# Kernel tuning notes

Hardware: AMD Instinct MI355X
Metric: run time of the kernel (lower is better)

The kernel has to match this reference:

```python
import jax, jax.numpy as jnp
import numpy as np

B, N, H, E, L = 64, 100, 128, 128, 3  # batch, nodes, node_hidden, edge_hidden, gcn layers


def setup_inputs() -> dict:
    key = jax.random.key(0)
    ks = jax.random.split(key, 12)
    s = 0.05
    return dict(
        node=jax.random.normal(ks[0], (B, N, 2), jnp.float32),
        demand=jax.random.uniform(ks[1], (B, N), jnp.float32),
        dis=jax.random.uniform(ks[2], (B, N, N), jnp.float32),
        Wn0=jax.random.normal(ks[3], (3, H), jnp.float32) * s,
        bn0=jnp.zeros((H,), jnp.float32),
        Ws=jax.random.normal(ks[4], (L, H, H), jnp.float32) * s,
        Wngh=jax.random.normal(ks[5], (L, H, H), jnp.float32) * s,
        We=jax.random.normal(ks[6], (E,), jnp.float32) * s,
        be=jnp.zeros((E,), jnp.float32),
        Wih=jax.random.normal(ks[7], (2, H, 3 * H), jnp.float32) * s,
        Whh=jax.random.normal(ks[8], (2, H, 3 * H), jnp.float32) * s,
        bih=jnp.zeros((2, 3 * H), jnp.float32),
        bhh=jnp.zeros((2, 3 * H), jnp.float32),
        Wq=jax.random.normal(ks[9], (H, H), jnp.float32) * s,
        Wc=jax.random.normal(ks[10], (E, 2), jnp.float32) * s,
        bc=jnp.zeros((2,), jnp.float32),
    )


def _gru(xin, h, Wih, Whh, bih, bhh):
    gi = xin @ Wih + bih
    gh = h @ Whh + bhh
    ir, iz, inn = jnp.split(gi, 3, -1)
    hr, hz, hn = jnp.split(gh, 3, -1)
    r = jax.nn.sigmoid(ir + hr)
    z = jax.nn.sigmoid(iz + hz)
    n = jnp.tanh(inn + r * hn)
    return (1.0 - z) * n + z * h


def _decode(x, Wih, Whh, bih, bhh, Wq, sample, key):
    b, n, h = x.shape
    scale = 1.0 / np.sqrt(h).astype(np.float32)

    def step(carry, _):
        last, hid, k = carry
        emb = x[jnp.arange(b), last]                      # [b,h]
        h0 = _gru(emb, hid[0], Wih[0], Whh[0], bih[0], bhh[0])
        h1 = _gru(h0, hid[1], Wih[1], Whh[1], bih[1], bhh[1])
        logits = jnp.einsum('bh,bnh->bn', h1 @ Wq, x) * scale
        logp = jax.nn.log_softmax(logits, -1)
        k, sk = jax.random.split(k)
        if sample:
            ind = jax.random.categorical(sk, logits)
        else:
            ind = jnp.argmax(logits, -1)
        ind = ind.astype(jnp.int32)
        chosen = jnp.take_along_axis(logp, ind[:, None], 1)[:, 0]
        return (ind, jnp.stack([h0, h1]), k), (ind, chosen)

    init = (jnp.zeros((b,), jnp.int32), jnp.zeros((2, b, h), x.dtype), key)
    _, (inds, lps) = jax.lax.scan(step, init, None, length=n - 1)
    solution = jnp.concatenate([jnp.zeros((b, 1), jnp.int32), inds.T], axis=1)  # depot 0 first
    return lps.T, solution  # logprob [b,n-1], solution [b,n]


def _count_dist(sol, dis):
    bidx = jnp.arange(sol.shape[0])[:, None]
    return dis[bidx, sol[:, :-1], sol[:, 1:]].sum(axis=1, keepdims=True)  # [b,1]


def reference(node, demand, dis, Wn0, bn0, Ws, Wngh, We, be, Wih, Whh, bih, bhh, Wq, Wc, bc):
    # --- GCN encoder ---
    h = jax.nn.relu(jnp.concatenate([node, demand[..., None]], -1) @ Wn0 + bn0)  # [B,N,H]
    A = jax.nn.softmax(-dis, -1)  # distance-based soft adjacency
    for l in range(Ws.shape[0]):
        h = jax.nn.relu(h @ Ws[l] + jnp.einsum('bij,bjh->bih', A, h @ Wngh[l]))
    e = jax.nn.relu(dis[..., None] * We + be)  # [B,N,N,E]

    key = jax.random.key(42)
    k1, _ = jax.random.split(key)
    sample_logprob, sample_solution = _decode(h, Wih, Whh, bih, bhh, Wq, True, k1)
    sample_distance = _count_dist(sample_solution, dis)
    _, greedy_solution = _decode(h, Wih, Whh, bih, bhh, Wq, False, k1)
    greedy_distance = _count_dist(greedy_solution, dis)

    predict_matrix = jax.nn.softmax(e @ Wc + bc, -1)  # [B,N,N,2]

    b, n = h.shape[0], h.shape[1]
    bidx = jnp.arange(b)[:, None]
    greedy_solution_matrix = (
        jnp.zeros((b, n, n), jnp.int32)
        .at[bidx, greedy_solution[:, :-1], greedy_solution[:, 1:]]
        .set(1)
    )
    return (sample_logprob, sample_distance, greedy_distance, predict_matrix, greedy_solution_matrix)
```

## Files before the change

### kernel.cpp

```cpp
#include <hip/hip_runtime.h>
#include <math.h>

#define BB 64
#define NN 100
#define HH 128
#define T3 384

#define O0 0
#define O1 6336
#define O2 6400
#define O3 6464
#define O4 1286464

#define TINYF 1.17549435e-38f

__device__ __forceinline__ unsigned rotl32(unsigned x, int d) {
    return (x << d) | (x >> (32 - d));
}

__device__ __forceinline__ void tf2x32(unsigned ks0, unsigned ks1,
                                       unsigned x0, unsigned x1,
                                       unsigned& o0, unsigned& o1) {
    unsigned ks2 = ks0 ^ ks1 ^ 0x1BD11BDAu;
    x0 += ks0; x1 += ks1;
    x0 += x1; x1 = rotl32(x1, 13); x1 ^= x0;
    x0 += x1; x1 = rotl32(x1, 15); x1 ^= x0;
    x0 += x1; x1 = rotl32(x1, 26); x1 ^= x0;
    x0 += x1; x1 = rotl32(x1, 6);  x1 ^= x0;
    x0 += ks1; x1 += ks2 + 1u;
    x0 += x1; x1 = rotl32(x1, 17); x1 ^= x0;
    x0 += x1; x1 = rotl32(x1, 29); x1 ^= x0;
    x0 += x1; x1 = rotl32(x1, 16); x1 ^= x0;
    x0 += x1; x1 = rotl32(x1, 24); x1 ^= x0;
    x0 += ks2; x1 += ks0 + 2u;
    x0 += x1; x1 = rotl32(x1, 13); x1 ^= x0;
    x0 += x1; x1 = rotl32(x1, 15); x1 ^= x0;
    x0 += x1; x1 = rotl32(x1, 26); x1 ^= x0;
    x0 += x1; x1 = rotl32(x1, 6);  x1 ^= x0;
    x0 += ks0; x1 += ks1 + 3u;
    x0 += x1; x1 = rotl32(x1, 17); x1 ^= x0;
    x0 += x1; x1 = rotl32(x1, 29); x1 ^= x0;
    x0 += x1; x1 = rotl32(x1, 16); x1 ^= x0;
    x0 += x1; x1 = rotl32(x1, 24); x1 ^= x0;
    x0 += ks1; x1 += ks2 + 4u;
    x0 += x1; x1 = rotl32(x1, 13); x1 ^= x0;
    x0 += x1; x1 = rotl32(x1, 15); x1 ^= x0;
    x0 += x1; x1 = rotl32(x1, 26); x1 ^= x0;
    x0 += x1; x1 = rotl32(x1, 6);  x1 ^= x0;
    x0 += ks2; x1 += ks0 + 5u;
    o0 = x0; o1 = x1;
}

__device__ __forceinline__ float gumbel_f(unsigned k0, unsigned k1, unsigned f) {
    unsigned o0, o1;
    tf2x32(k0, k1, 0u, f, o0, o1);
    unsigned bits = o0 ^ o1;
    float u01 = __uint_as_float((bits >> 9) | 0x3F800000u) - 1.0f;
    float u = fmaxf(TINYF, u01 * (1.0f - TINYF) + TINYF);
    return -logf(-logf(u));
}


__global__ void k_embed(const float* __restrict__ node, const float* __restrict__ demand,
                        const float* __restrict__ Wn0, const float* __restrict__ bn0,
                        float* __restrict__ h) {
    int idx = blockIdx.x * 256 + threadIdx.x;
    if (idx >= BB * NN * HH) return;
    int r = idx >> 7, c = idx & 127;
    float v = node[r * 2] * Wn0[c] + node[r * 2 + 1] * Wn0[128 + c]
            + demand[r] * Wn0[256 + c] + bn0[c];
    h[idx] = fmaxf(v, 0.0f);
}

__global__ void k_adj(const float* __restrict__ dis, float* __restrict__ A) {
    int row = blockIdx.x;
    const float* d = dis + row * NN;
    int l = threadIdx.x;
    float v0 = (l < NN) ? -d[l] : -__builtin_inff();
    float v1 = (l + 64 < NN) ? -d[l + 64] : -__builtin_inff();
    float m = fmaxf(v0, v1);
    for (int off = 32; off > 0; off >>= 1) m = fmaxf(m, __shfl_xor(m, off));
    float e0 = (l < NN) ? expf(v0 - m) : 0.0f;
    float e1 = (l + 64 < NN) ? expf(v1 - m) : 0.0f;
    float s = e0 + e1;
    for (int off = 32; off > 0; off >>= 1) s += __shfl_xor(s, off);
    float inv = 1.0f / s;
    if (l < NN) A[row * NN + l] = e0 * inv;
    if (l + 64 < NN) A[row * NN + l + 64] = e1 * inv;
}

__global__ void k_hw(const float* __restrict__ h, const float* __restrict__ W,
                     float* __restrict__ out) {
    __shared__ float hs[8 * 128];
    int block_row = blockIdx.x * 8;
    int tid = threadIdx.x;
    int col = tid & 127;
    int rg = tid >> 7;
    for (int i = tid; i < 8 * 128; i += 256) hs[i] = h[block_row * 128 + i];
    __syncthreads();
    float acc[4] = {0.f, 0.f, 0.f, 0.f};
    for (int k = 0; k < 128; k++) {
        float w = W[k * 128 + col];
#pragma unroll
        for (int r = 0; r < 4; r++) acc[r] += hs[(rg + 2 * r) * 128 + k] * w;
    }
#pragma unroll
    for (int r = 0; r < 4; r++)
        out[(block_row + rg + 2 * r) * 128 + col] = acc[r];
}

__global__ void k_mm384(const float* __restrict__ h, const float* __restrict__ W,
                        const float* __restrict__ bias, float* __restrict__ out) {
    __shared__ float hs[8 * 128];
    int block_row = blockIdx.x * 8;
    int tid = threadIdx.x;
    int col = blockIdx.y * 128 + (tid & 127);
    int rg = tid >> 7;
    for (int i = tid; i < 8 * 128; i += 256) hs[i] = h[block_row * 128 + i];
    __syncthreads();
    float acc[4] = {0.f, 0.f, 0.f, 0.f};
    for (int k = 0; k < 128; k++) {
        float w = W[k * 384 + col];
#pragma unroll
        for (int r = 0; r < 4; r++) acc[r] += hs[(rg + 2 * r) * 128 + k] * w;
    }
    float b = bias[col];
#pragma unroll
    for (int r = 0; r < 4; r++)
        out[(block_row + rg + 2 * r) * 384 + col] = acc[r] + b;
}

__global__ void k_transpose128(const float* __restrict__ Wq, float* __restrict__ WqT) {
    int i = blockIdx.x * 256 + threadIdx.x;
    if (i >= 128 * 128) return;
    int k = i >> 7, c = i & 127;
    WqT[k * 128 + c] = Wq[c * 128 + k];
}

__global__ void k_agg(const float* __restrict__ h, const float* __restrict__ Ws,
                      const float* __restrict__ A, const float* __restrict__ hw,
                      float* __restrict__ out) {
    __shared__ float hs[4 * 128];
    __shared__ float As[4 * 100];
    int b = blockIdx.x / 25;
    int i0 = (blockIdx.x % 25) * 4;
    int tid = threadIdx.x;
    int col = tid & 127;
    int rg = tid >> 7;
    int rowbase = b * NN + i0;
    for (int idx = tid; idx < 4 * 128; idx += 256) hs[idx] = h[rowbase * 128 + idx];
    for (int idx = tid; idx < 4 * 100; idx += 256) As[idx] = A[rowbase * 100 + idx];
    __syncthreads();
    float acc0 = 0.f, acc1 = 0.f;
    for (int k = 0; k < 128; k++) {
        float w = Ws[k * 128 + col];
        acc0 += hs[rg * 128 + k] * w;
        acc1 += hs[(rg + 2) * 128 + k] * w;
    }
    const float* hwb = hw + b * NN * 128;
    for (int j = 0; j < NN; j++) {
        float v = hwb[j * 128 + col];
        acc0 += As[rg * 100 + j] * v;
        acc1 += As[(rg + 2) * 100 + j] * v;
    }
    out[(rowbase + rg) * 128 + col]     = fmaxf(acc0, 0.0f);
    out[(rowbase + rg + 2) * 128 + col] = fmaxf(acc1, 0.0f);
}

__global__ void k_predict(const float* __restrict__ dis, const float* __restrict__ We,
                          const float* __restrict__ be, const float* __restrict__ Wc,
                          const float* __restrict__ bc, float* __restrict__ out3) {
    __shared__ float sWe[128], sbe[128], sc0[128], sc1[128];
    int tid = threadIdx.x;
    if (tid < 128) {
        sWe[tid] = We[tid];
        sbe[tid] = be[tid];
        sc0[tid] = Wc[tid * 2];
        sc1[tid] = Wc[tid * 2 + 1];
    }
    __syncthreads();
    float b0 = bc[0], b1 = bc[1];
    for (int pos = blockIdx.x * 256 + tid; pos < BB * NN * NN; pos += gridDim.x * 256) {
        float d = dis[pos];
        float a0 = b0, a1 = b1;
        for (int k = 0; k < 128; k++) {
            float e = fmaxf(d * sWe[k] + sbe[k], 0.0f);
            a0 += e * sc0[k];
            a1 += e * sc1[k];
        }
        float m = fmaxf(a0, a1);
        float p0 = expf(a0 - m), p1 = expf(a1 - m);
        float inv = 1.0f / (p0 + p1);
        out3[pos * 2]     = p0 * inv;
        out3[pos * 2 + 1] = p1 * inv;
    }
}

__global__ void k_zero(float* __restrict__ p, int n) {
    int i = blockIdx.x * 256 + threadIdx.x;
    if (i < n) p[i] = 0.0f;
}

__global__ __launch_bounds__(768) void k_decode2(
    const float* __restrict__ P0,
    const float* __restrict__ Z,
    const float* __restrict__ dis,
    const float* __restrict__ Wih,
    const float* __restrict__ Whh,
    const float* __restrict__ bih,
    const float* __restrict__ bhh,
    float* __restrict__ out) {
    __shared__ float Zs[NN * 129];
    __shared__ float h0s[128], h1s[128];
    __shared__ float gi0s[T3];
    __shared__ float pg0[2 * T3];
    __shared__ float gi1s[T3], gh1s[T3];
    __shared__ float sbhh0[T3], sbih1[T3], sbhh1[T3];
    __shared__ float pl[4 * NN];
    __shared__ float logits[NN];
    __shared__ float s_m, s_s;
    __shared__ int s_ind;

    const int tid = threadIdx.x;
    const int b = blockIdx.x >> 1;
    const int greedy = blockIdx.x & 1;
    const float SCALE = 0.08838834764831845f;

    const float* Whh0 = Whh;
    const float* Wih1 = Wih + 128 * T3;
    const float* Whh1 = Whh + 128 * T3;

    for (int idx = tid; idx < NN * 128; idx += 768) {
        int r = idx >> 7, c = idx & 127;
        Zs[r * 129 + c] = Z[(b * NN + r) * 128 + c];
    }
    if (tid < T3) {
        sbhh0[tid] = bhh[tid];
        sbih1[tid] = bih[T3 + tid];
        sbhh1[tid] = bhh[T3 + tid];
    }
    if (tid < 128) { h0s[tid] = 0.0f; h1s[tid] = 0.0f; }

    unsigned kk0, kk1;
    tf2x32(0u, 42u, 0u, 0u, kk0, kk1);

    int last = 0;
    float dist = 0.0f;
    __syncthreads();

    for (int t = 0; t < NN - 1; t++) {
        unsigned sk0, sk1, nk0, nk1;
        tf2x32(kk0, kk1, 0u, 1u, sk0, sk1);
        tf2x32(kk0, kk1, 0u, 0u, nk0, nk1);
        kk0 = nk0; kk1 = nk1;

        {
            const float* P0row = P0 + (b * NN + last) * T3;
            if (tid < T3) {
                int j = tid;
                float acc = 0.0f;
#pragma unroll 16
                for (int k = 0; k < 64; k++) acc += h0s[k] * Whh0[k * T3 + j];
                pg0[j] = acc;
                gi0s[j] = P0row[j];
            } else {
                int j = tid - T3;
                float acc = 0.0f;
#pragma unroll 16
                for (int k = 64; k < 128; k++) acc += h0s[k] * Whh0[k * T3 + j];
                pg0[T3 + j] = acc;
            }
        }
        __syncthreads();

        if (tid < 128) {
            float ghr = pg0[tid] + pg0[T3 + tid] + sbhh0[tid];
            float ghz = pg0[tid + 128] + pg0[T3 + tid + 128] + sbhh0[tid + 128];
            float ghn = pg0[tid + 256] + pg0[T3 + tid + 256] + sbhh0[tid + 256];
            float r = 1.0f / (1.0f + expf(-(gi0s[tid] + ghr)));
            float z = 1.0f / (1.0f + expf(-(gi0s[tid + 128] + ghz)));
            float n = tanhf(gi0s[tid + 256] + r * ghn);
            h0s[tid] = (1.0f - z) * n + z * h0s[tid];
        }
        __syncthreads();

        if (tid < T3) {
            int j = tid;
            float acc = sbih1[j];
#pragma unroll 16
            for (int k = 0; k < 128; k++) acc += h0s[k] * Wih1[k * T3 + j];
            gi1s[j] = acc;
        } else {
            int j = tid - T3;
            float acc = sbhh1[j];
#pragma unroll 16
            for (int k = 0; k < 128; k++) acc += h1s[k] * Whh1[k * T3 + j];
            gh1s[j] = acc;
        }
        __syncthreads();

        if (tid < 128) {
            float r = 1.0f / (1.0f + expf(-(gi1s[tid] + gh1s[tid])));
            float z = 1.0f / (1.0f + expf(-(gi1s[tid + 128] + gh1s[tid + 128])));
            float n = tanhf(gi1s[tid + 256] + r * gh1s[tid + 256]);
            h1s[tid] = (1.0f - z) * n + z * h1s[tid];
        }
        __syncthreads();

        if (tid < 400) {
            int n = tid % 100, p = tid / 100;
            int k0 = p * 32;
            float acc = 0.0f;
#pragma unroll
            for (int kk = 0; kk < 32; kk++) acc += h1s[k0 + kk] * Zs[n * 129 + k0 + kk];
            pl[p * 100 + n] = acc;
        }
        __syncthreads();

        if (tid < 64) {
            float v0 = -__builtin_inff(), v1 = -__builtin_inff();
            {
                int n = tid;
                v0 = (pl[n] + pl[100 + n] + pl[200 + n] + pl[300 + n]) * SCALE;
                logits[n] = v0;
            }
            if (tid + 64 < NN) {
                int n = tid + 64;
                v1 = (pl[n] + pl[100 + n] + pl[200 + n] + pl[300 + n]) * SCALE;
                logits[n] = v1;
            }
            float m = fmaxf(v0, v1);
            for (int off = 32; off > 0; off >>= 1) m = fmaxf(m, __shfl_xor(m, off));
            float e = expf(v0 - m) + ((tid + 64 < NN) ? expf(v1 - m) : 0.0f);
            for (int off = 32; off > 0; off >>= 1) e += __shfl_xor(e, off);
            float a0 = v0, a1 = v1;
            if (!greedy) {
                a0 = v0 + gumbel_f(sk0, sk1, (unsigned)(b * NN + tid));
                if (tid + 64 < NN) a1 = v1 + gumbel_f(sk0, sk1, (unsigned)(b * NN + tid + 64));
            }
            float bv; int bi;
            if (a1 > a0) { bv = a1; bi = tid + 64; } else { bv = a0; bi = tid; }
            for (int off = 32; off > 0; off >>= 1) {
                float ov = __shfl_xor(bv, off);
                int   oi = __shfl_xor(bi, off);
                if (ov > bv || (ov == bv && oi < bi)) { bv = ov; bi = oi; }
            }
            if (tid == 0) { s_m = m; s_s = e; s_ind = bi; }
        }
        __syncthreads();
        int ind = s_ind;
        if (tid == 0) {
            if (!greedy) out[O0 + b * (NN - 1) + t] = logits[ind] - s_m - logf(s_s);
            dist += dis[b * NN * NN + last * NN + ind];
            if (greedy) out[O4 + b * NN * NN + last * NN + ind] = 1.0f;
        }
        last = ind;
        __syncthreads();
    }
    if (tid == 0) {
        if (!greedy) out[O1 + b] = dist;
        else         out[O2 + b] = dist;
    }
}

__device__ __forceinline__ void gru_layer(const float* __restrict__ xin,
                                          float* __restrict__ hstate,
                                          const float* __restrict__ Wih,
                                          const float* __restrict__ Whh,
                                          const float* __restrict__ bih,
                                          const float* __restrict__ bhh,
                                          float* gi, float* gh, int tid) {
    for (int j = tid; j < T3; j += 256) {
        float ai = bih[j], ah = bhh[j];
        const float* wi = Wih + j;
        const float* wh = Whh + j;
        for (int k = 0; k < 128; k++) {
            ai += xin[k] * wi[k * T3];
            ah += hstate[k] * wh[k * T3];
        }
        gi[j] = ai; gh[j] = ah;
    }
    __syncthreads();
    if (tid < 128) {
        float r = 1.0f / (1.0f + expf(-(gi[tid] + gh[tid])));
        float z = 1.0f / (1.0f + expf(-(gi[128 + tid] + gh[128 + tid])));
        float n = tanhf(gi[256 + tid] + r * gh[256 + tid]);
        hstate[tid] = (1.0f - z) * n + z * hstate[tid];
    }
    __syncthreads();
}

__global__ __launch_bounds__(256) void k_decode(
    const float* __restrict__ x, const float* __restrict__ dis,
    const float* __restrict__ Wih, const float* __restrict__ Whh,
    const float* __restrict__ bih, const float* __restrict__ bhh,
    const float* __restrict__ Wq, float* __restrict__ out) {
    __shared__ float xs[NN * 129];
    __shared__ float h0[128], h1[128];
    __shared__ float gi[T3], gh[T3];
    __shared__ float q[128];
    __shared__ float logits[NN];
    __shared__ float s_m, s_s;
    __shared__ int s_ind;

    const int tid = threadIdx.x;
    const int b = blockIdx.x >> 1;
    const int greedy = blockIdx.x & 1;
    const float SCALE = 0.08838834764831845f;

    for (int idx = tid; idx < NN * 128; idx += 256) {
        int r = idx >> 7, c = idx & 127;
        xs[r * 129 + c] = x[(b * NN + r) * 128 + c];
    }
    if (tid < 128) { h0[tid] = 0.0f; h1[tid] = 0.0f; }

    unsigned kk0, kk1;
    tf2x32(0u, 42u, 0u, 0u, kk0, kk1);

    int last = 0;
    float dist = 0.0f;
    __syncthreads();

    for (int t = 0; t < NN - 1; t++) {
        unsigned sk0, sk1, nk0, nk1;
        tf2x32(kk0, kk1, 0u, 1u, sk0, sk1);
        tf2x32(kk0, kk1, 0u, 0u, nk0, nk1);
        kk0 = nk0; kk1 = nk1;

        gru_layer(&xs[last * 129], h0, Wih, Whh, bih, bhh, gi, gh, tid);
        gru_layer(h0, h1, Wih + 128 * T3, Whh + 128 * T3, bih + T3, bhh + T3, gi, gh, tid);

        if (tid < 128) {
            float acc = 0.0f;
            for (int k = 0; k < 128; k++) acc += h1[k] * Wq[k * 128 + tid];
            q[tid] = acc;
        }
        __syncthreads();
        if (tid < NN) {
            float acc = 0.0f;
            for (int k = 0; k < 128; k++) acc += q[k] * xs[tid * 129 + k];
            logits[tid] = acc * SCALE;
        }
        __syncthreads();
        if (tid < 64) {
            float v0 = (tid < NN) ? logits[tid] : -__builtin_inff();
            float v1 = (tid + 64 < NN) ? logits[tid + 64] : -__builtin_inff();
            float m = fmaxf(v0, v1);
            for (int off = 32; off > 0; off >>= 1) m = fmaxf(m, __shfl_xor(m, off));
            float e = ((tid < NN) ? expf(v0 - m) : 0.0f)
                    + ((tid + 64 < NN) ? expf(v1 - m) : 0.0f);
            for (int off = 32; off > 0; off >>= 1) e += __shfl_xor(e, off);
            float a0 = v0, a1 = v1;
            if (!greedy) {
                if (tid < NN)      a0 = v0 + gumbel_f(sk0, sk1, (unsigned)(b * NN + tid));
                if (tid + 64 < NN) a1 = v1 + gumbel_f(sk0, sk1, (unsigned)(b * NN + tid + 64));
            }
            float bv; int bi;
            if (a1 > a0) { bv = a1; bi = tid + 64; } else { bv = a0; bi = tid; }
            for (int off = 32; off > 0; off >>= 1) {
                float ov = __shfl_xor(bv, off);
                int   oi = __shfl_xor(bi, off);
                if (ov > bv || (ov == bv && oi < bi)) { bv = ov; bi = oi; }
            }
            if (tid == 0) { s_m = m; s_s = e; s_ind = bi; }
        }
        __syncthreads();
        int ind = s_ind;
        if (tid == 0) {
            if (!greedy) out[O0 + b * (NN - 1) + t] = logits[ind] - s_m - logf(s_s);
            dist += dis[b * NN * NN + last * NN + ind];
            if (greedy) out[O4 + b * NN * NN + last * NN + ind] = 1.0f;
        }
        last = ind;
        __syncthreads();
    }
    if (tid == 0) {
        if (!greedy) out[O1 + b] = dist;
        else         out[O2 + b] = dist;
    }
}

extern "C" void kernel_launch(void* const* d_in, const int* in_sizes, int n_in,
                              void* d_out, int out_size, void* d_ws, size_t ws_size,
                              hipStream_t stream) {
    (void)in_sizes; (void)n_in; (void)out_size;
    const float* node   = (const float*)d_in[0];
    const float* demand = (const float*)d_in[1];
    const float* dis    = (const float*)d_in[2];
    const float* Wn0    = (const float*)d_in[3];
    const float* bn0    = (const float*)d_in[4];
    const float* Ws     = (const float*)d_in[5];
    const float* Wngh   = (const float*)d_in[6];
    const float* We     = (const float*)d_in[7];
    const float* be     = (const float*)d_in[8];
    const float* Wih    = (const float*)d_in[9];
    const float* Whh    = (const float*)d_in[10];
    const float* bih    = (const float*)d_in[11];
    const float* bhh    = (const float*)d_in[12];
    const float* Wq     = (const float*)d_in[13];
    const float* Wc     = (const float*)d_in[14];
    const float* bc     = (const float*)d_in[15];
    float* out = (float*)d_out;
    float* ws  = (float*)d_ws;

    float* hA  = ws;
    float* hB  = ws + 819200;
    float* hw  = ws + 1638400;
    float* A   = ws + 2457600;
    float* P0  = ws + 2457600;
    float* WqT = ws + 4915200;
    const size_t need_bytes = (size_t)4931584 * 4;
    const bool big_ws = ws_size >= need_bytes;

    hipLaunchKernelGGL(k_embed, dim3(3200), dim3(256), 0, stream, node, demand, Wn0, bn0, hA);
    hipLaunchKernelGGL(k_adj, dim3(6400), dim3(64), 0, stream, dis, A);

    float* cur = hA;
    float* nxt = hB;
    for (int l = 0; l < 3; l++) {
        hipLaunchKernelGGL(k_hw, dim3(800), dim3(256), 0, stream, cur, Wngh + l * 16384, hw);
        hipLaunchKernelGGL(k_agg, dim3(1600), dim3(256), 0, stream, cur, Ws + l * 16384, A, hw, nxt);
        float* tswap = cur; cur = nxt; nxt = tswap;
    }

    hipLaunchKernelGGL(k_predict, dim3(2500), dim3(256), 0, stream, dis, We, be, Wc, bc, out + O3);
    hipLaunchKernelGGL(k_zero, dim3(2500), dim3(256), 0, stream, out + O4, BB * NN * NN);

    if (big_ws) {
        hipLaunchKernelGGL(k_transpose128, dim3(64), dim3(256), 0, stream, Wq, WqT);
        hipLaunchKernelGGL(k_hw, dim3(800), dim3(256), 0, stream, cur, WqT, hw);
        hipLaunchKernelGGL(k_mm384, dim3(800, 3), dim3(256), 0, stream, cur, Wih, bih, P0);
        hipLaunchKernelGGL(k_decode2, dim3(128), dim3(768), 0, stream,
                           P0, hw, dis, Wih, Whh, bih, bhh, out);
    } else {
        hipLaunchKernelGGL(k_decode, dim3(128), dim3(256), 0, stream,
                           cur, dis, Wih, Whh, bih, bhh, Wq, out);
    }
}
```

Before: 1.054 ms.

## Fuse sample and greedy decodes into one block with register-tiled GRU matvecs

Adds a k_decode3 kernel in which each block decodes both the sampled and the greedy trajectory for one batch element, so every GRU weight element is loaded once and applied to two hidden states. The matvecs are register-tiled, with each thread computing an 8- or 4-wide output chunk over a k-slice using float4 weight loads, and the hidden states are replicated in shared memory to reduce bank conflicts. Gumbel noise generation is overlapped with the Whh matvec. The trade-off is half as many blocks (64), and higher register and shared-memory use per block. The old k_decode fallback is removed, and the else branch now duplicates the precompute path and uses k_decode2.

```diff
diff --git a/kernel.cpp b/kernel.cpp
--- a/kernel.cpp
+++ b/kernel.cpp
@@ -13,6 +13,7 @@
 #define O4 1286464
 
 #define TINYF 1.17549435e-38f
+#define SCALEF 0.08838834764831845f
 
 __device__ __forceinline__ unsigned rotl32(unsigned x, int d) {
     return (x << d) | (x >> (32 - d));
@@ -201,7 +202,7 @@
     if (i < n) p[i] = 0.0f;
 }
 
-__global__ __launch_bounds__(768) void k_decode2(
+__global__ __launch_bounds__(768, 3) void k_decode3(
     const float* __restrict__ P0,
     const float* __restrict__ Z,
     const float* __restrict__ dis,
@@ -210,13 +211,272 @@
     const float* __restrict__ bih,
     const float* __restrict__ bhh,
     float* __restrict__ out) {
+    __shared__ float Zs[NN * 132];
+    __shared__ float hrep0[8 * 2 * 140];
+    __shared__ float hrep1[8 * 2 * 140];
+    __shared__ float gi0s[2 * 384];
+    __shared__ float pgA[2 * 4 * 2 * 392];
+    __shared__ float pgC[8 * 2 * 392];
+    __shared__ float sbhh0[T3], sbih1[T3], sbhh1[T3];
+    __shared__ float pl[2 * 4 * 100];
+    __shared__ float gum[128];
+    __shared__ int s_ind2[2];
+
+    const int tid = threadIdx.x;
+    const int b = blockIdx.x;
+
+    for (int i4 = tid; i4 < NN * 32; i4 += 768) {
+        int r = i4 >> 5, c4 = (i4 & 31) * 4;
+        *(float4*)&Zs[r * 132 + c4] = *(const float4*)&Z[(b * NN + r) * 128 + c4];
+    }
+    if (tid < T3) {
+        sbhh0[tid] = bhh[tid];
+        sbih1[tid] = bih[T3 + tid];
+        sbhh1[tid] = bhh[T3 + tid];
+    }
+    if (tid < 256) {
+        int m = tid >> 7, i = tid & 127;
+#pragma unroll
+        for (int rep = 0; rep < 8; rep++) {
+            hrep0[(rep * 2 + m) * 140 + i] = 0.0f;
+            hrep1[(rep * 2 + m) * 140 + i] = 0.0f;
+        }
+    }
+    if (tid == 0) { s_ind2[0] = 0; s_ind2[1] = 0; }
+
+    unsigned kk0, kk1;
+    tf2x32(0u, 42u, 0u, 0u, kk0, kk1);
+
+    int lastm = 0;
+    float dist = 0.0f;
+    __syncthreads();
+
+    for (int t = 0; t < NN - 1; t++) {
+        if (tid < 384) {
+            const int unit = tid / 192;
+            const int r = tid % 192;
+            const int jg = r >> 2, ks = r & 3;
+            const int j0 = jg * 8, k0 = ks * 32;
+            const float* __restrict__ W = Whh + unit * 128 * T3;
+            const float* __restrict__ hsrc = (unit == 0) ? hrep0 : hrep1;
+            float a[2][8];
+#pragma unroll
+            for (int m = 0; m < 2; m++)
+#pragma unroll
+                for (int j = 0; j < 8; j++) a[m][j] = 0.0f;
+#pragma unroll
+            for (int half = 0; half < 2; half++) {
+                const int kb = k0 + half * 16;
+                float hh0[16], hh1[16];
+#pragma unroll
+                for (int q = 0; q < 4; q++) {
+                    float4 v0 = *(const float4*)&hsrc[(ks * 2 + 0) * 140 + kb + 4 * q];
+                    float4 v1 = *(const float4*)&hsrc[(ks * 2 + 1) * 140 + kb + 4 * q];
+                    hh0[4*q] = v0.x; hh0[4*q+1] = v0.y; hh0[4*q+2] = v0.z; hh0[4*q+3] = v0.w;
+                    hh1[4*q] = v1.x; hh1[4*q+1] = v1.y; hh1[4*q+2] = v1.z; hh1[4*q+3] = v1.w;
+                }
+#pragma unroll
+                for (int kk = 0; kk < 16; kk++) {
+                    float4 w0 = *(const float4*)&W[(kb + kk) * T3 + j0];
+                    float4 w1 = *(const float4*)&W[(kb + kk) * T3 + j0 + 4];
+                    float x0 = hh0[kk], x1 = hh1[kk];
+                    a[0][0] += w0.x * x0; a[0][1] += w0.y * x0;
+                    a[0][2] += w0.z * x0; a[0][3] += w0.w * x0;
+                    a[0][4] += w1.x * x0; a[0][5] += w1.y * x0;
+                    a[0][6] += w1.z * x0; a[0][7] += w1.w * x0;
+                    a[1][0] += w0.x * x1; a[1][1] += w0.y * x1;
+                    a[1][2] += w0.z * x1; a[1][3] += w0.w * x1;
+                    a[1][4] += w1.x * x1; a[1][5] += w1.y * x1;
+                    a[1][6] += w1.z * x1; a[1][7] += w1.w * x1;
+                }
+            }
+#pragma unroll
+            for (int m = 0; m < 2; m++) {
+                int base = ((unit * 4 + ks) * 2 + m) * 392 + j0;
+                float4 o;
+                o.x = a[m][0]; o.y = a[m][1]; o.z = a[m][2]; o.w = a[m][3];
+                *(float4*)&pgA[base] = o;
+                o.x = a[m][4]; o.y = a[m][5]; o.z = a[m][6]; o.w = a[m][7];
+                *(float4*)&pgA[base + 4] = o;
+            }
+        } else {
+            int u = tid - 384;
+            int m = u / 192, j2 = (u % 192) * 2;
+            int lastv = s_ind2[m];
+            float2 g2 = *(const float2*)&P0[(size_t)(b * NN + lastv) * T3 + j2];
+            gi0s[m * 384 + j2] = g2.x;
+            gi0s[m * 384 + j2 + 1] = g2.y;
+            if (tid < 448) {
+                unsigned sk0, sk1, nk0, nk1;
+                tf2x32(kk0, kk1, 0u, 1u, sk0, sk1);
+                tf2x32(kk0, kk1, 0u, 0u, nk0, nk1);
+                kk0 = nk0; kk1 = nk1;
+                int lane = tid & 63;
+                gum[lane] = gumbel_f(sk0, sk1, (unsigned)(b * NN + lane));
+                if (lane + 64 < NN)
+                    gum[lane + 64] = gumbel_f(sk0, sk1, (unsigned)(b * NN + lane + 64));
+            }
+        }
+        __syncthreads();
+
+        if (tid < 256) {
+            int m = tid >> 7, i = tid & 127;
+            float ghr = 0.f, ghz = 0.f, ghn = 0.f;
+#pragma unroll
+            for (int ks = 0; ks < 4; ks++) {
+                int pb = (ks * 2 + m) * 392;
+                ghr += pgA[pb + i];
+                ghz += pgA[pb + i + 128];
+                ghn += pgA[pb + i + 256];
+            }
+            ghr += sbhh0[i]; ghz += sbhh0[i + 128]; ghn += sbhh0[i + 256];
+            float rr = 1.0f / (1.0f + expf(-(gi0s[m * 384 + i] + ghr)));
+            float zz = 1.0f / (1.0f + expf(-(gi0s[m * 384 + i + 128] + ghz)));
+            float nn = tanhf(gi0s[m * 384 + i + 256] + rr * ghn);
+            float hold = hrep0[m * 140 + i];
+            float hnew = (1.0f - zz) * nn + zz * hold;
+#pragma unroll
+            for (int rep = 0; rep < 8; rep++) hrep0[(rep * 2 + m) * 140 + i] = hnew;
+        }
+        __syncthreads();
+
+        {
+            const int jg = tid >> 3, ks = tid & 7;
+            const int j0 = jg * 4, k0 = ks * 16;
+            const float* __restrict__ W = Wih + 128 * T3;
+            float hh0[16], hh1[16];
+#pragma unroll
+            for (int q = 0; q < 4; q++) {
+                float4 v0 = *(const float4*)&hrep0[(ks * 2 + 0) * 140 + k0 + 4 * q];
+                float4 v1 = *(const float4*)&hrep0[(ks * 2 + 1) * 140 + k0 + 4 * q];
+                hh0[4*q] = v0.x; hh0[4*q+1] = v0.y; hh0[4*q+2] = v0.z; hh0[4*q+3] = v0.w;
+                hh1[4*q] = v1.x; hh1[4*q+1] = v1.y; hh1[4*q+2] = v1.z; hh1[4*q+3] = v1.w;
+            }
+            float a0[4] = {0.f,0.f,0.f,0.f}, a1[4] = {0.f,0.f,0.f,0.f};
+#pragma unroll
+            for (int kk = 0; kk < 16; kk++) {
+                float4 w = *(const float4*)&W[(k0 + kk) * T3 + j0];
+                a0[0] += w.x * hh0[kk]; a0[1] += w.y * hh0[kk];
+                a0[2] += w.z * hh0[kk]; a0[3] += w.w * hh0[kk];
+                a1[0] += w.x * hh1[kk]; a1[1] += w.y * hh1[kk];
+                a1[2] += w.z * hh1[kk]; a1[3] += w.w * hh1[kk];
+            }
+            float4 o;
+            o.x = a0[0]; o.y = a0[1]; o.z = a0[2]; o.w = a0[3];
+            *(float4*)&pgC[(ks * 2 + 0) * 392 + j0] = o;
+            o.x = a1[0]; o.y = a1[1]; o.z = a1[2]; o.w = a1[3];
+            *(float4*)&pgC[(ks * 2 + 1) * 392 + j0] = o;
+        }
+        __syncthreads();
+
+        if (tid < 256) {
+            int m = tid >> 7, i = tid & 127;
+            float gir = 0.f, giz = 0.f, gin = 0.f;
+#pragma unroll
+            for (int ks = 0; ks < 8; ks++) {
+                int pb = (ks * 2 + m) * 392;
+                gir += pgC[pb + i];
+                giz += pgC[pb + i + 128];
+                gin += pgC[pb + i + 256];
+            }
+            gir += sbih1[i]; giz += sbih1[i + 128]; gin += sbih1[i + 256];
+            float ghr = 0.f, ghz = 0.f, ghn = 0.f;
+#pragma unroll
+            for (int ks = 0; ks < 4; ks++) {
+                int pb = ((4 + ks) * 2 + m) * 392;
+                ghr += pgA[pb + i];
+                ghz += pgA[pb + i + 128];
+                ghn += pgA[pb + i + 256];
+            }
+            ghr += sbhh1[i]; ghz += sbhh1[i + 128]; ghn += sbhh1[i + 256];
+            float rr = 1.0f / (1.0f + expf(-(gir + ghr)));
+            float zz = 1.0f / (1.0f + expf(-(giz + ghz)));
+            float nn = tanhf(gin + rr * ghn);
+            float hold = hrep1[m * 140 + i];
+            float hnew = (1.0f - zz) * nn + zz * hold;
+#pragma unroll
+            for (int rep = 0; rep < 8; rep++) hrep1[(rep * 2 + m) * 140 + i] = hnew;
+        }
+        __syncthreads();
+
+        if (tid < 400) {
+            int p = tid / 100, n = tid % 100;
+            int k0 = p * 32;
+            float a0 = 0.f, a1 = 0.f;
+#pragma unroll
+            for (int q = 0; q < 8; q++) {
+                float4 zz = *(const float4*)&Zs[n * 132 + k0 + 4 * q];
+                float4 h0v = *(const float4*)&hrep1[(p * 2 + 0) * 140 + k0 + 4 * q];
+                float4 h1v = *(const float4*)&hrep1[(p * 2 + 1) * 140 + k0 + 4 * q];
+                a0 += h0v.x * zz.x; a0 += h0v.y * zz.y; a0 += h0v.z * zz.z; a0 += h0v.w * zz.w;
+                a1 += h1v.x * zz.x; a1 += h1v.y * zz.y; a1 += h1v.z * zz.z; a1 += h1v.w * zz.w;
+            }
+            pl[(0 * 4 + p) * 100 + n] = a0;
+            pl[(1 * 4 + p) * 100 + n] = a1;
+        }
+        __syncthreads();
+
+        if (tid < 128) {
+            const int m = tid >> 6, lane = tid & 63;
+            float v0, v1 = -__builtin_inff();
+            {
+                int n = lane;
+                v0 = (pl[(m * 4 + 0) * 100 + n] + pl[(m * 4 + 1) * 100 + n]
+                    + pl[(m * 4 + 2) * 100 + n] + pl[(m * 4 + 3) * 100 + n]) * SCALEF;
+            }
+            if (lane + 64 < NN) {
+                int n = lane + 64;
+                v1 = (pl[(m * 4 + 0) * 100 + n] + pl[(m * 4 + 1) * 100 + n]
+                    + pl[(m * 4 + 2) * 100 + n] + pl[(m * 4 + 3) * 100 + n]) * SCALEF;
+            }
+            float mx = fmaxf(v0, v1);
+            for (int off = 32; off > 0; off >>= 1) mx = fmaxf(mx, __shfl_xor(mx, off));
+            float e = expf(v0 - mx) + ((lane + 64 < NN) ? expf(v1 - mx) : 0.0f);
+            for (int off = 32; off > 0; off >>= 1) e += __shfl_xor(e, off);
+            float a0 = v0, a1 = v1;
+            if (m == 0) {
+                a0 += gum[lane];
+                if (lane + 64 < NN) a1 += gum[lane + 64];
+            }
+            float bv; int bi;
+            if (a1 > a0) { bv = a1; bi = lane + 64; } else { bv = a0; bi = lane; }
+            for (int off = 32; off > 0; off >>= 1) {
+                float ov = __shfl_xor(bv, off);
+                int   oi = __shfl_xor(bi, off);
+                if (ov > bv || (ov == bv && oi < bi)) { bv = ov; bi = oi; }
+            }
+            int ind = bi;
+            float la = __shfl(v0, ind & 63);
+            float lb = __shfl(v1, ind & 63);
+            float lv = (ind < 64) ? la : lb;
+            if (lane == 0) {
+                if (m == 0) out[O0 + b * (NN - 1) + t] = lv - mx - logf(e);
+                else        out[O4 + (size_t)b * NN * NN + lastm * NN + ind] = 1.0f;
+                s_ind2[m] = ind;
+            }
+            dist += dis[b * NN * NN + lastm * NN + ind];
+            lastm = ind;
+        }
+        __syncthreads();
+    }
+
+    if (tid == 0)  out[O1 + b] = dist;
+    if (tid == 64) out[O2 + b] = dist;
+}
+
+__global__ __launch_bounds__(768) void k_decode2(
+    const float* __restrict__ P0, const float* __restrict__ Z,
+    const float* __restrict__ dis,
+    const float* __restrict__ Wih, const float* __restrict__ Whh,
+    const float* __restrict__ bih, const float* __restrict__ bhh,
+    float* __restrict__ out) {
     __shared__ float Zs[NN * 129];
     __shared__ float h0s[128], h1s[128];
     __shared__ float gi0s[T3];
     __shared__ float pg0[2 * T3];
     __shared__ float gi1s[T3], gh1s[T3];
     __shared__ float sbhh0[T3], sbih1[T3], sbhh1[T3];
-    __shared__ float pl[4 * NN];
+    __shared__ float plx[4 * NN];
     __shared__ float logits[NN];
     __shared__ float s_m, s_s;
     __shared__ int s_ind;
@@ -224,7 +484,6 @@
     const int tid = threadIdx.x;
     const int b = blockIdx.x >> 1;
     const int greedy = blockIdx.x & 1;
-    const float SCALE = 0.08838834764831845f;
 
     const float* Whh0 = Whh;
     const float* Wih1 = Wih + 128 * T3;
@@ -255,24 +514,21 @@
         kk0 = nk0; kk1 = nk1;
 
         {
-            const float* P0row = P0 + (b * NN + last) * T3;
+            const float* P0row = P0 + (size_t)(b * NN + last) * T3;
             if (tid < T3) {
                 int j = tid;
                 float acc = 0.0f;
-#pragma unroll 16
                 for (int k = 0; k < 64; k++) acc += h0s[k] * Whh0[k * T3 + j];
                 pg0[j] = acc;
                 gi0s[j] = P0row[j];
             } else {
                 int j = tid - T3;
                 float acc = 0.0f;
-#pragma unroll 16
                 for (int k = 64; k < 128; k++) acc += h0s[k] * Whh0[k * T3 + j];
                 pg0[T3 + j] = acc;
             }
         }
         __syncthreads();
-
         if (tid < 128) {
             float ghr = pg0[tid] + pg0[T3 + tid] + sbhh0[tid];
             float ghz = pg0[tid + 128] + pg0[T3 + tid + 128] + sbhh0[tid + 128];
@@ -283,22 +539,18 @@
             h0s[tid] = (1.0f - z) * n + z * h0s[tid];
         }
         __syncthreads();
-
         if (tid < T3) {
             int j = tid;
             float acc = sbih1[j];
-#pragma unroll 16
             for (int k = 0; k < 128; k++) acc += h0s[k] * Wih1[k * T3 + j];
             gi1s[j] = acc;
         } else {
             int j = tid - T3;
             float acc = sbhh1[j];
-#pragma unroll 16
             for (int k = 0; k < 128; k++) acc += h1s[k] * Whh1[k * T3 + j];
             gh1s[j] = acc;
         }
         __syncthreads();
-
         if (tid < 128) {
             float r = 1.0f / (1.0f + expf(-(gi1s[tid] + gh1s[tid])));
             float z = 1.0f / (1.0f + expf(-(gi1s[tid + 128] + gh1s[tid + 128])));
@@ -306,27 +558,24 @@
             h1s[tid] = (1.0f - z) * n + z * h1s[tid];
         }
         __syncthreads();
-
         if (tid < 400) {
             int n = tid % 100, p = tid / 100;
             int k0 = p * 32;
             float acc = 0.0f;
-#pragma unroll
             for (int kk = 0; kk < 32; kk++) acc += h1s[k0 + kk] * Zs[n * 129 + k0 + kk];
-            pl[p * 100 + n] = acc;
-        }
-        __syncthreads();
-
+            plx[p * 100 + n] = acc;
+        }
+        __syncthreads();
         if (tid < 64) {
             float v0 = -__builtin_inff(), v1 = -__builtin_inff();
             {
                 int n = tid;
-                v0 = (pl[n] + pl[100 + n] + pl[200 + n] + pl[300 + n]) * SCALE;
+                v0 = (plx[n] + plx[100 + n] + plx[200 + n] + plx[300 + n]) * SCALEF;
                 logits[n] = v0;
             }
             if (tid + 64 < NN) {
                 int n = tid + 64;
-                v1 = (pl[n] + pl[100 + n] + pl[200 + n] + pl[300 + n]) * SCALE;
+                v1 = (plx[n] + plx[100 + n] + plx[200 + n] + plx[300 + n]) * SCALEF;
                 logits[n] = v1;
             }
             float m = fmaxf(v0, v1);
@@ -336,123 +585,6 @@
             float a0 = v0, a1 = v1;
             if (!greedy) {
                 a0 = v0 + gumbel_f(sk0, sk1, (unsigned)(b * NN + tid));
-                if (tid + 64 < NN) a1 = v1 + gumbel_f(sk0, sk1, (unsigned)(b * NN + tid + 64));
-            }
-            float bv; int bi;
-            if (a1 > a0) { bv = a1; bi = tid + 64; } else { bv = a0; bi = tid; }
-            for (int off = 32; off > 0; off >>= 1) {
-                float ov = __shfl_xor(bv, off);
-                int   oi = __shfl_xor(bi, off);
-                if (ov > bv || (ov == bv && oi < bi)) { bv = ov; bi = oi; }
-            }
-            if (tid == 0) { s_m = m; s_s = e; s_ind = bi; }
-        }
-        __syncthreads();
-        int ind = s_ind;
-        if (tid == 0) {
-            if (!greedy) out[O0 + b * (NN - 1) + t] = logits[ind] - s_m - logf(s_s);
-            dist += dis[b * NN * NN + last * NN + ind];
-            if (greedy) out[O4 + b * NN * NN + last * NN + ind] = 1.0f;
-        }
-        last = ind;
-        __syncthreads();
-    }
-    if (tid == 0) {
-        if (!greedy) out[O1 + b] = dist;
-        else         out[O2 + b] = dist;
-    }
-}
-
-__device__ __forceinline__ void gru_layer(const float* __restrict__ xin,
-                                          float* __restrict__ hstate,
-                                          const float* __restrict__ Wih,
-                                          const float* __restrict__ Whh,
-                                          const float* __restrict__ bih,
-                                          const float* __restrict__ bhh,
-                                          float* gi, float* gh, int tid) {
-    for (int j = tid; j < T3; j += 256) {
-        float ai = bih[j], ah = bhh[j];
-        const float* wi = Wih + j;
-        const float* wh = Whh + j;
-        for (int k = 0; k < 128; k++) {
-            ai += xin[k] * wi[k * T3];
-            ah += hstate[k] * wh[k * T3];
-        }
-        gi[j] = ai; gh[j] = ah;
-    }
-    __syncthreads();
-    if (tid < 128) {
-        float r = 1.0f / (1.0f + expf(-(gi[tid] + gh[tid])));
-        float z = 1.0f / (1.0f + expf(-(gi[128 + tid] + gh[128 + tid])));
-        float n = tanhf(gi[256 + tid] + r * gh[256 + tid]);
-        hstate[tid] = (1.0f - z) * n + z * hstate[tid];
-    }
-    __syncthreads();
-}
-
-__global__ __launch_bounds__(256) void k_decode(
-    const float* __restrict__ x, const float* __restrict__ dis,
-    const float* __restrict__ Wih, const float* __restrict__ Whh,
-    const float* __restrict__ bih, const float* __restrict__ bhh,
-    const float* __restrict__ Wq, float* __restrict__ out) {
-    __shared__ float xs[NN * 129];
-    __shared__ float h0[128], h1[128];
-    __shared__ float gi[T3], gh[T3];
-    __shared__ float q[128];
-    __shared__ float logits[NN];
-    __shared__ float s_m, s_s;
-    __shared__ int s_ind;
-
-    const int tid = threadIdx.x;
-    const int b = blockIdx.x >> 1;
-    const int greedy = blockIdx.x & 1;
-    const float SCALE = 0.08838834764831845f;
-
-    for (int idx = tid; idx < NN * 128; idx += 256) {
-        int r = idx >> 7, c = idx & 127;
-        xs[r * 129 + c] = x[(b * NN + r) * 128 + c];
-    }
-    if (tid < 128) { h0[tid] = 0.0f; h1[tid] = 0.0f; }
-
-    unsigned kk0, kk1;
-    tf2x32(0u, 42u, 0u, 0u, kk0, kk1);
-
-    int last = 0;
-    float dist = 0.0f;
-    __syncthreads();
-
-    for (int t = 0; t < NN - 1; t++) {
-        unsigned sk0, sk1, nk0, nk1;
-        tf2x32(kk0, kk1, 0u, 1u, sk0, sk1);
-        tf2x32(kk0, kk1, 0u, 0u, nk0, nk1);
-        kk0 = nk0; kk1 = nk1;
-
-        gru_layer(&xs[last * 129], h0, Wih, Whh, bih, bhh, gi, gh, tid);
-        gru_layer(h0, h1, Wih + 128 * T3, Whh + 128 * T3, bih + T3, bhh + T3, gi, gh, tid);
-
-        if (tid < 128) {
-            float acc = 0.0f;
-            for (int k = 0; k < 128; k++) acc += h1[k] * Wq[k * 128 + tid];
-            q[tid] = acc;
-        }
-        __syncthreads();
-        if (tid < NN) {
-            float acc = 0.0f;
-            for (int k = 0; k < 128; k++) acc += q[k] * xs[tid * 129 + k];
-            logits[tid] = acc * SCALE;
-        }
-        __syncthreads();
-        if (tid < 64) {
-            float v0 = (tid < NN) ? logits[tid] : -__builtin_inff();
-            float v1 = (tid + 64 < NN) ? logits[tid + 64] : -__builtin_inff();
-            float m = fmaxf(v0, v1);
-            for (int off = 32; off > 0; off >>= 1) m = fmaxf(m, __shfl_xor(m, off));
-            float e = ((tid < NN) ? expf(v0 - m) : 0.0f)
-                    + ((tid + 64 < NN) ? expf(v1 - m) : 0.0f);
-            for (int off = 32; off > 0; off >>= 1) e += __shfl_xor(e, off);
-            float a0 = v0, a1 = v1;
-            if (!greedy) {
-                if (tid < NN)      a0 = v0 + gumbel_f(sk0, sk1, (unsigned)(b * NN + tid));
                 if (tid + 64 < NN) a1 = v1 + gumbel_f(sk0, sk1, (unsigned)(b * NN + tid + 64));
             }
             float bv; int bi;
@@ -530,10 +662,13 @@
         hipLaunchKernelGGL(k_transpose128, dim3(64), dim3(256), 0, stream, Wq, WqT);
         hipLaunchKernelGGL(k_hw, dim3(800), dim3(256), 0, stream, cur, WqT, hw);
         hipLaunchKernelGGL(k_mm384, dim3(800, 3), dim3(256), 0, stream, cur, Wih, bih, P0);
+        hipLaunchKernelGGL(k_decode3, dim3(64), dim3(768), 0, stream,
+                           P0, hw, dis, Wih, Whh, bih, bhh, out);
+    } else {
+        hipLaunchKernelGGL(k_transpose128, dim3(64), dim3(256), 0, stream, Wq, WqT);
+        hipLaunchKernelGGL(k_hw, dim3(800), dim3(256), 0, stream, cur, WqT, hw);
+        hipLaunchKernelGGL(k_mm384, dim3(800, 3), dim3(256), 0, stream, cur, Wih, bih, P0);
         hipLaunchKernelGGL(k_decode2, dim3(128), dim3(768), 0, stream,
                            P0, hw, dis, Wih, Whh, bih, bhh, out);
-    } else {
-        hipLaunchKernelGGL(k_decode, dim3(128), dim3(256), 0, stream,
-                           cur, dis, Wih, Whh, bih, bhh, Wq, out);
-    }
-}
+    }
+}
```

New measurement: 2.249 ms. +113.3%, slower.
